# Performance work log

Measured on AMD Instinct MI355X. Metric: run time of the kernel, lower is better.

The kernel has to match this reference:

```python
import jax, jax.numpy as jnp
import numpy as np

B, T_HIST, D, H, STEPS = 2048, 15, 64, 128, 20
MAX_STEPS = 48           # max adaptive steps per unit time interval
DT0, RTOL, ATOL = 0.1, 1e-3, 1e-6
SAFETY, FMIN, FMAX = 0.9, 0.2, 10.0

# Tsit5 (Tsitouras 2011) tableau
A21 = 0.161
A31, A32 = -0.008480655492356989, 0.335480655492357
A41, A42, A43 = 2.8971530571054935, -6.359448489975075, 4.3622954328695815
A51, A52, A53, A54 = 5.325864828439257, -11.748883564062828, 7.4955393428898365, -0.09249506636175525
A61, A62, A63, A64, A65 = 5.86145544294642, -12.92096931784711, 8.159367898576159, -0.071584973281401, -0.028269050394068383
B1, B2, B3, B4, B5, B6 = 0.09646076681806523, 0.01, 0.4798896504144996, 1.379008574103742, -3.290069515436081, 2.324710524099774
E1, E2, E3, E4, E5, E6, E7 = (-0.00178001105222577714, -0.0008164344596567469, 0.007880878010261995,
                              -0.1447110071732629, 0.5823571654525552, -0.45808210592918697, 0.015151515151515152)


def _mlp(y, W1, b1, W2, b2, W3, b3):
    h = jax.nn.softplus(y @ W1.T + b1)
    h = jax.nn.softplus(h @ W2.T + b2)
    return h @ W3.T + b3


def _solve(y0, W1, b1, W2, b2, W3, b3, steps):
    f = lambda y: _mlp(y, W1, b1, W2, b2, W3, b3)  # batched vector field [B,D]->[B,D]
    Bn = y0.shape[0]

    def segment(carry, t1):
        y, dt = carry
        t = jnp.full((Bn,), t1 - 1.0, y0.dtype)
        done = jnp.zeros((Bn,), bool)

        def body(state, _):
            t, y, dt, done = state
            dt_c = jnp.minimum(dt, t1 - t)          # clip to segment end
            h = dt_c[:, None]
            k1 = f(y)
            k2 = f(y + h * (A21 * k1))
            k3 = f(y + h * (A31 * k1 + A32 * k2))
            k4 = f(y + h * (A41 * k1 + A42 * k2 + A43 * k3))
            k5 = f(y + h * (A51 * k1 + A52 * k2 + A53 * k3 + A54 * k4))
            k6 = f(y + h * (A61 * k1 + A62 * k2 + A63 * k3 + A64 * k4 + A65 * k5))
            y5 = y + h * (B1 * k1 + B2 * k2 + B3 * k3 + B4 * k4 + B5 * k5 + B6 * k6)
            k7 = f(y5)
            err = h * (E1 * k1 + E2 * k2 + E3 * k3 + E4 * k4 + E5 * k5 + E6 * k6 + E7 * k7)
            scale = ATOL + RTOL * jnp.maximum(jnp.abs(y), jnp.abs(y5))
            err_norm = jnp.sqrt(jnp.mean((err / scale) ** 2, axis=-1))  # [B]
            accept = (err_norm <= 1.0) & (~done)
            factor = jnp.clip(SAFETY * jnp.maximum(err_norm, 1e-10) ** (-0.2), FMIN, FMAX)
            t_new = jnp.where(accept, t + dt_c, t)
            y_new = jnp.where(accept[:, None], y5, y)
            dt_new = jnp.where(done, dt, dt_c * factor)
            done_new = done | (t_new >= t1 - 1e-8)
            return (t_new, y_new, dt_new, done_new), None

        (t, y, dt, done), _ = jax.lax.scan(jax.checkpoint(body), (t, y, dt, done), None, length=MAX_STEPS)
        return (y, dt), y

    ts1 = jnp.arange(1, steps + 1, dtype=y0.dtype)
    dt0 = jnp.full((Bn,), DT0, y0.dtype)
    (_, _), ys = jax.lax.scan(segment, (y0, dt0), ts1)  # ys: [steps, B, D]
    return jnp.transpose(ys, (1, 0, 2))                  # [B, steps, D]


def setup_inputs() -> dict:
    key = jax.random.key(0)
    ks = jax.random.split(key, 7)
    history = jax.random.normal(ks[0], (B, T_HIST, D), jnp.float32)
    # small-scale init keeps the vector field mild so adaptive steps converge
    W1 = jax.random.normal(ks[1], (H, D), jnp.float32) * (0.5 / np.sqrt(D))
    b1 = jax.random.normal(ks[2], (H,), jnp.float32) * 0.05
    W2 = jax.random.normal(ks[3], (H, H), jnp.float32) * (0.5 / np.sqrt(H))
    b2 = jax.random.normal(ks[4], (H,), jnp.float32) * 0.05
    W3 = jax.random.normal(ks[5], (D, H), jnp.float32) * (0.1 / np.sqrt(H))
    b3 = jax.random.normal(ks[6], (D,), jnp.float32) * 0.05
    return {"history": history, "W1": W1, "b1": b1, "W2": W2, "b2": b2, "W3": W3, "b3": b3, "steps": STEPS}


def reference(history, W1, b1, W2, b2, W3, b3, steps):
    y0 = history[:, -1]  # NeuralODE uses only the last history state
    return _solve(y0, W1, b1, W2, b2, W3, b3, steps)
```

## Files before the change

kernel.cpp:

```cpp
#include <hip/hip_runtime.h>
#include <math.h>

#define NB    2048
#define NSEG  20
#define MAXIT 48
#define CH    544
#define BLKS  136

typedef __attribute__((ext_vector_type(8))) short bf8_t;
typedef __attribute__((ext_vector_type(4))) float f32x4;

#define cA21 ((float)0.161)
#define cA31 ((float)-0.008480655492356989)
#define cA32 ((float)0.335480655492357)
#define cA41 ((float)2.8971530571054935)
#define cA42 ((float)-6.359448489975075)
#define cA43 ((float)4.3622954328695815)
#define cA51 ((float)5.325864828439257)
#define cA52 ((float)-11.748883564062828)
#define cA53 ((float)7.4955393428898365)
#define cA54 ((float)-0.09249506636175525)
#define cA61 ((float)5.86145544294642)
#define cA62 ((float)-12.92096931784711)
#define cA63 ((float)8.159367898576159)
#define cA64 ((float)-0.071584973281401)
#define cA65 ((float)-0.028269050394068383)
#define cB1  ((float)0.09646076681806523)
#define cB2  ((float)0.01)
#define cB3  ((float)0.4798896504144996)
#define cB4  ((float)1.379008574103742)
#define cB5  ((float)-3.290069515436081)
#define cB6  ((float)2.324710524099774)
#define cE1  ((float)-0.001780011052225777)
#define cE2  ((float)-0.0008164344596567469)
#define cE3  ((float)0.007880878010261995)
#define cE4  ((float)-0.1447110071732629)
#define cE5  ((float)0.5823571654525552)
#define cE6  ((float)-0.45808210592918697)
#define cE7  ((float)0.015151515151515152)

__device__ __forceinline__ void split2(float x, short &hi, short &lo) {
    unsigned u = __float_as_uint(x);
    hi = (short)(u >> 16);
    float r = x - __uint_as_float(u & 0xFFFF0000u);
    lo = (short)(__float_as_uint(r) >> 16);
}

__device__ __forceinline__ float softplus_f(float x) {
    float t = exp2f(-fabsf(x) * 1.442695040888963f);
    return fmaxf(x, 0.0f) + log2f(1.0f + t) * 0.6931471805599453f;
}

__device__ __forceinline__ unsigned pk(short a, short b) {
    return ((unsigned)(unsigned short)a) | (((unsigned)(unsigned short)b) << 16);
}

__device__ __forceinline__ float fold8(float x) {
    int r = __builtin_amdgcn_update_dpp(__float_as_int(x), __float_as_int(x),
                                        0x128, 0xF, 0xF, false);
    return x + __int_as_float(r);
}

__global__ __launch_bounds__(512)
void ode_kernel(const float* __restrict__ history,
                const float* __restrict__ W1, const float* __restrict__ b1,
                const float* __restrict__ W2, const float* __restrict__ b2,
                const float* __restrict__ W3, const float* __restrict__ b3,
                float* __restrict__ out)
{
    __shared__ alignas(16) short argB[2 * CH];
    __shared__ alignas(16) short h1B[4 * CH];
    __shared__ alignas(16) short h2B[4 * CH];
    __shared__ float rrP[32];

    const int tid  = threadIdx.x;
    const int wave = tid >> 6, lane = tid & 63;
    const int quad = lane >> 4, col = lane & 15;
    const int jb   = 16 * wave + 4 * quad;

    bf8_t A1h[2], A1l[2], A2h[4], A2l[4], A3h[4], A3l[4];
#pragma unroll
    for (int c = 0; c < 2; ++c) {
        const float* p = W1 + (size_t)(16 * wave + col) * 64 + 32 * c + 8 * quad;
        bf8_t h, l;
#pragma unroll
        for (int j = 0; j < 8; ++j) { short hs, ls; split2(p[j], hs, ls); h[j] = hs; l[j] = ls; }
        A1h[c] = h; A1l[c] = l;
    }
#pragma unroll
    for (int c = 0; c < 4; ++c) {
        const float* p = W2 + (size_t)(16 * wave + col) * 128 + 32 * c + 8 * quad;
        bf8_t h, l;
#pragma unroll
        for (int j = 0; j < 8; ++j) { short hs, ls; split2(p[j], hs, ls); h[j] = hs; l[j] = ls; }
        A2h[c] = h; A2l[c] = l;
    }
    const int esel = col >> 3;
    const int e    = col & 7;
    const int d0   = 16 * wave + 4 * quad + 2 * esel;
    const size_t elemIdx = (size_t)(blockIdx.x * 8 + e);

    float b3v0 = 0.f, b3v1 = 0.f;
    if (wave < 4) {
#pragma unroll
        for (int c = 0; c < 4; ++c) {
            const float* p = W3 + (size_t)(16 * wave + col) * 128 + 32 * c + 8 * quad;
            bf8_t h, l;
#pragma unroll
            for (int j = 0; j < 8; ++j) { short hs, ls; split2(p[j], hs, ls); h[j] = hs; l[j] = ls; }
            A3h[c] = h; A3l[c] = l;
        }
        b3v0 = b3[d0]; b3v1 = b3[d0 + 1];
    } else {
        bf8_t z = {0, 0, 0, 0, 0, 0, 0, 0};
#pragma unroll
        for (int c = 0; c < 4; ++c) { A3h[c] = z; A3l[c] = z; }
    }
    const f32x4 b1f = *(const f32x4*)(b1 + jb);
    const f32x4 b2f = *(const f32x4*)(b2 + jb);

    const int ai = (d0 >> 5) * CH + ((d0 >> 3) & 3) * BLKS + e * 8 + (d0 & 7);

    const int j0    = 16 * wave + 4 * quad + 2 * esel;
    const int epidx = (j0 >> 5) * CH + ((j0 >> 3) & 3) * BLKS + e * 8 + (j0 & 7);

    const int boff = quad * BLKS + col * 8;

    auto gemm = [&](const bf8_t* Ah, const bf8_t* Al, const short* Bc, int nch) -> f32x4 {
        f32x4 a0 = {0.f, 0.f, 0.f, 0.f}, a1 = a0;
#pragma unroll
        for (int c = 0; c < nch; ++c) {
            bf8_t b = *(const bf8_t*)(Bc + c * CH + boff);
            a0 = __builtin_amdgcn_mfma_f32_16x16x32_bf16(Ah[c], b, a0, 0, 0, 0);
            a1 = __builtin_amdgcn_mfma_f32_16x16x32_bf16(Al[c], b, a1, 0, 0, 0);
        }
        f32x4 s;
#pragma unroll
        for (int r = 0; r < 4; ++r) s[r] = a0[r] + a1[r];
        return s;
    };

    auto epi = [&](f32x4 s, f32x4 bias, short* Bn) {
        float t0 = fold8(s[0]) + bias[0];
        float t1 = fold8(s[1]) + bias[1];
        float t2 = fold8(s[2]) + bias[2];
        float t3 = fold8(s[3]) + bias[3];
        float x0 = esel ? t2 : t0;
        float x1 = esel ? t3 : t1;
        float p0 = softplus_f(x0), p1 = softplus_f(x1);
        short h0, l0, h1, l1;
        split2(p0, h0, l0);
        split2(p1, h1, l1);
        *(unsigned*)(Bn + epidx)      = pk(h0, h1);
        *(unsigned*)(Bn + epidx + 64) = pk(l0, l1);
    };

    auto eval = [&](float &kv0, float &kv1) {
        __syncthreads();
        f32x4 s1 = gemm(A1h, A1l, argB, 2);
        epi(s1, b1f, h1B);
        __syncthreads();
        f32x4 s2 = gemm(A2h, A2l, h1B, 4);
        epi(s2, b2f, h2B);
        __syncthreads();
        if (wave < 4) {
            f32x4 s3 = gemm(A3h, A3l, h2B, 4);
            float f0 = fold8(s3[0]);
            float f1 = fold8(s3[1]);
            float f2 = fold8(s3[2]);
            float f3 = fold8(s3[3]);
            kv0 = (esel ? f2 : f0) + b3v0;
            kv1 = (esel ? f3 : f1) + b3v1;
        }
    };

    float y0 = 0.f, y1 = 0.f;
    float dt = 0.1f;
    float k1a = 0.f, k1b = 0.f, k2a, k2b, k3a, k3b, k4a, k4b, k5a, k5b, k6a, k6b;

    if (wave < 4) {
        float2 yy = *(const float2*)(history + (elemIdx * 15 + 14) * 64 + d0);
        y0 = yy.x; y1 = yy.y;
        short h0, l0, h1, l1;
        split2(y0, h0, l0); split2(y1, h1, l1);
        *(unsigned*)(argB + ai)      = pk(h0, h1);
        *(unsigned*)(argB + ai + 64) = pk(l0, l1);
    }
    eval(k1a, k1b);

#pragma unroll 1
    for (int seg = 1; seg <= NSEG; ++seg) {
        const float t1 = (float)seg;
        float t = t1 - 1.0f;
        bool done = false;

#pragma unroll 1
        for (int it = 0; it < MAXIT; ++it) {
            const float dt_c = fminf(dt, t1 - t);
            const float h = dt_c;
            float y50 = 0.f, y51 = 0.f, k7a = 0.f, k7b = 0.f;

#pragma unroll 1
            for (int st = 2; st <= 7; ++st) {
                if (wave < 4) {
                    float sum0, sum1;
                    switch (st) {
                        case 2: sum0 = cA21 * k1a;
                                sum1 = cA21 * k1b; break;
                        case 3: sum0 = fmaf(cA31, k1a, cA32 * k2a);
                                sum1 = fmaf(cA31, k1b, cA32 * k2b); break;
                        case 4: sum0 = fmaf(cA41, k1a, fmaf(cA42, k2a, cA43 * k3a));
                                sum1 = fmaf(cA41, k1b, fmaf(cA42, k2b, cA43 * k3b)); break;
                        case 5: sum0 = fmaf(cA51, k1a, fmaf(cA52, k2a, fmaf(cA53, k3a, cA54 * k4a)));
                                sum1 = fmaf(cA51, k1b, fmaf(cA52, k2b, fmaf(cA53, k3b, cA54 * k4b))); break;
                        case 6: sum0 = fmaf(cA61, k1a, fmaf(cA62, k2a, fmaf(cA63, k3a, fmaf(cA64, k4a, cA65 * k5a))));
                                sum1 = fmaf(cA61, k1b, fmaf(cA62, k2b, fmaf(cA63, k3b, fmaf(cA64, k4b, cA65 * k5b)))); break;
                        default: sum0 = fmaf(cB1, k1a, fmaf(cB2, k2a, fmaf(cB3, k3a, fmaf(cB4, k4a, fmaf(cB5, k5a, cB6 * k6a)))));
                                 sum1 = fmaf(cB1, k1b, fmaf(cB2, k2b, fmaf(cB3, k3b, fmaf(cB4, k4b, fmaf(cB5, k5b, cB6 * k6b))))); break;
                    }
                    float arg0 = fmaf(h, sum0, y0);
                    float arg1 = fmaf(h, sum1, y1);
                    if (st == 7) { y50 = arg0; y51 = arg1; }
                    short h0, l0, h1, l1;
                    split2(arg0, h0, l0); split2(arg1, h1, l1);
                    *(unsigned*)(argB + ai)      = pk(h0, h1);
                    *(unsigned*)(argB + ai + 64) = pk(l0, l1);
                }
                float kv0 = 0.f, kv1 = 0.f;
                eval(kv0, kv1);
                if (wave < 4) {
                    switch (st) {
                        case 2: k2a = kv0; k2b = kv1; break;
                        case 3: k3a = kv0; k3b = kv1; break;
                        case 4: k4a = kv0; k4b = kv1; break;
                        case 5: k5a = kv0; k5b = kv1; break;
                        case 6: k6a = kv0; k6b = kv1; break;
                        default: k7a = kv0; k7b = kv1; break;
                    }
                }
            }

            float rr2 = 0.f;
            if (wave < 4) {
                float es0 = fmaf(cE1, k1a, fmaf(cE2, k2a, fmaf(cE3, k3a,
                            fmaf(cE4, k4a, fmaf(cE5, k5a, fmaf(cE6, k6a, cE7 * k7a))))));
                float es1 = fmaf(cE1, k1b, fmaf(cE2, k2b, fmaf(cE3, k3b,
                            fmaf(cE4, k4b, fmaf(cE5, k5b, fmaf(cE6, k6b, cE7 * k7b))))));
                float err0 = h * es0, err1 = h * es1;
                float sc0 = fmaf(1e-3f, fmaxf(fabsf(y0), fabsf(y50)), 1e-6f);
                float sc1 = fmaf(1e-3f, fmaxf(fabsf(y1), fabsf(y51)), 1e-6f);
                float r0 = err0 / sc0, r1 = err1 / sc1;
                rr2 = fmaf(r0, r0, r1 * r1);
            }
            rr2 += __shfl_xor(rr2, 16, 64);
            rr2 += __shfl_xor(rr2, 32, 64);
            rr2 = fold8(rr2);
            if (wave < 4 && lane < 8) rrP[wave * 8 + lane] = rr2;
            __syncthreads();
            float rs = ((rrP[e] + rrP[8 + e]) + rrP[16 + e]) + rrP[24 + e];
            float en = sqrtf(rs * (1.0f / 64.0f));

            bool accept = (en <= 1.0f) && !done;
            float fac = 0.9f * exp2f(-0.2f * log2f(fmaxf(en, 1e-10f)));
            fac = fminf(fmaxf(fac, 0.2f), 10.0f);

            if (wave < 4 && accept) { y0 = y50; y1 = y51; k1a = k7a; k1b = k7b; }
            if (accept) t += dt_c;
            if (!done) dt = dt_c * fac;
            done = done || (t >= t1 - 1e-8f);
            if (__all(done)) break;
        }

        if (wave < 4) {
            float2 yy; yy.x = y0; yy.y = y1;
            *(float2*)(out + (elemIdx * NSEG + (seg - 1)) * 64 + d0) = yy;
        }
    }
}

extern "C" void kernel_launch(void* const* d_in, const int* in_sizes, int n_in,
                              void* d_out, int out_size, void* d_ws, size_t ws_size,
                              hipStream_t stream) {
    const float* history = (const float*)d_in[0];
    const float* W1 = (const float*)d_in[1];
    const float* b1 = (const float*)d_in[2];
    const float* W2 = (const float*)d_in[3];
    const float* b2 = (const float*)d_in[4];
    const float* W3 = (const float*)d_in[5];
    const float* b3 = (const float*)d_in[6];
    float* out = (float*)d_out;

    ode_kernel<<<dim3(NB / 8), dim3(512), 0, stream>>>(history, W1, b1, W2, b2, W3, b3, out);
}
```

Measured before the change: 278.7 us.

## Fold first-layer GEMM into last layer via precomputed W1·W3 product

```diff
diff --git a/kernel.cpp b/kernel.cpp
--- a/kernel.cpp
+++ b/kernel.cpp
@@ -68,7 +68,6 @@
                 const float* __restrict__ W3, const float* __restrict__ b3,
                 float* __restrict__ out)
 {
-    __shared__ alignas(16) short argB[2 * CH];
     __shared__ alignas(16) short h1B[4 * CH];
     __shared__ alignas(16) short h2B[4 * CH];
     __shared__ float rrP[32];
@@ -77,16 +76,14 @@
     const int wave = tid >> 6, lane = tid & 63;
     const int quad = lane >> 4, col = lane & 15;
     const int jb   = 16 * wave + 4 * quad;
-
-    bf8_t A1h[2], A1l[2], A2h[4], A2l[4], A3h[4], A3l[4];
-#pragma unroll
-    for (int c = 0; c < 2; ++c) {
-        const float* p = W1 + (size_t)(16 * wave + col) * 64 + 32 * c + 8 * quad;
-        bf8_t h, l;
-#pragma unroll
-        for (int j = 0; j < 8; ++j) { short hs, ls; split2(p[j], hs, ls); h[j] = hs; l[j] = ls; }
-        A1h[c] = h; A1l[c] = l;
-    }
+    const int esel = col >> 3;
+    const int e    = col & 7;
+    const int j0   = jb + 2 * esel;
+    const size_t elemIdx = (size_t)(blockIdx.x * 8 + e);
+    const int zi   = (j0 >> 5) * CH + ((j0 >> 3) & 3) * BLKS + e * 8 + (j0 & 7);
+    const int boff = quad * BLKS + col * 8;
+
+    bf8_t A2h[4], A2l[4];
 #pragma unroll
     for (int c = 0; c < 4; ++c) {
         const float* p = W2 + (size_t)(16 * wave + col) * 128 + 32 * c + 8 * quad;
@@ -95,11 +92,7 @@
         for (int j = 0; j < 8; ++j) { short hs, ls; split2(p[j], hs, ls); h[j] = hs; l[j] = ls; }
         A2h[c] = h; A2l[c] = l;
     }
-    const int esel = col >> 3;
-    const int e    = col & 7;
-    const int d0   = 16 * wave + 4 * quad + 2 * esel;
-    const size_t elemIdx = (size_t)(blockIdx.x * 8 + e);
-
+    bf8_t A3h[4], A3l[4];
     float b3v0 = 0.f, b3v1 = 0.f;
     if (wave < 4) {
 #pragma unroll
@@ -110,21 +103,46 @@
             for (int j = 0; j < 8; ++j) { short hs, ls; split2(p[j], hs, ls); h[j] = hs; l[j] = ls; }
             A3h[c] = h; A3l[c] = l;
         }
-        b3v0 = b3[d0]; b3v1 = b3[d0 + 1];
+        b3v0 = b3[j0]; b3v1 = b3[j0 + 1];
     } else {
         bf8_t z = {0, 0, 0, 0, 0, 0, 0, 0};
 #pragma unroll
         for (int c = 0; c < 4; ++c) { A3h[c] = z; A3l[c] = z; }
     }
-    const f32x4 b1f = *(const f32x4*)(b1 + jb);
     const f32x4 b2f = *(const f32x4*)(b2 + jb);
-
-    const int ai = (d0 >> 5) * CH + ((d0 >> 3) & 3) * BLKS + e * 8 + (d0 & 7);
-
-    const int j0    = 16 * wave + 4 * quad + 2 * esel;
-    const int epidx = (j0 >> 5) * CH + ((j0 >> 3) & 3) * BLKS + e * 8 + (j0 & 7);
-
-    const int boff = quad * BLKS + col * 8;
+    const float b1v0 = b1[j0], b1v1 = b1[j0 + 1];
+
+    bf8_t Mh[4], Ml[4];
+    {
+        float accM[4][8];
+#pragma unroll
+        for (int cc = 0; cc < 4; ++cc)
+#pragma unroll
+            for (int j = 0; j < 8; ++j) accM[cc][j] = 0.f;
+        const float* w1r = W1 + (size_t)(16 * wave + col) * 64;
+#pragma unroll 2
+        for (int d = 0; d < 64; ++d) {
+            float wv = w1r[d];
+            const float* w3r = W3 + (size_t)d * 128 + 8 * quad;
+#pragma unroll
+            for (int cc = 0; cc < 4; ++cc) {
+                f32x4 va = *(const f32x4*)(w3r + 32 * cc);
+                f32x4 vb = *(const f32x4*)(w3r + 32 * cc + 4);
+#pragma unroll
+                for (int j = 0; j < 4; ++j) {
+                    accM[cc][j]     = fmaf(wv, va[j], accM[cc][j]);
+                    accM[cc][4 + j] = fmaf(wv, vb[j], accM[cc][4 + j]);
+                }
+            }
+        }
+#pragma unroll
+        for (int cc = 0; cc < 4; ++cc) {
+            bf8_t hh, ll;
+#pragma unroll
+            for (int j = 0; j < 8; ++j) { short hs, ls; split2(accM[cc][j], hs, ls); hh[j] = hs; ll[j] = ls; }
+            Mh[cc] = hh; Ml[cc] = ll;
+        }
+    }
 
     auto gemm = [&](const bf8_t* Ah, const bf8_t* Al, const short* Bc, int nch) -> f32x4 {
         f32x4 a0 = {0.f, 0.f, 0.f, 0.f}, a1 = a0;
@@ -139,6 +157,41 @@
         for (int r = 0; r < 4; ++r) s[r] = a0[r] + a1[r];
         return s;
     };
+
+    float zy0, zy1, cc0, cc1;
+    float ys0 = 0.f, ys1 = 0.f;
+    {
+        bf8_t W1h[2], W1l[2];
+#pragma unroll
+        for (int c = 0; c < 2; ++c) {
+            const float* p = W1 + (size_t)(16 * wave + col) * 64 + 32 * c + 8 * quad;
+            bf8_t h, l;
+#pragma unroll
+            for (int j = 0; j < 8; ++j) { short hs, ls; split2(p[j], hs, ls); h[j] = hs; l[j] = ls; }
+            W1h[c] = h; W1l[c] = l;
+        }
+        if (wave < 4) {
+            float2 yy = *(const float2*)(history + (elemIdx * 15 + 14) * 64 + j0);
+            ys0 = yy.x; ys1 = yy.y;
+            short ha, la, hb, lb;
+            split2(ys0, ha, la); split2(ys1, hb, lb);
+            *(unsigned*)(h1B + zi)      = pk(ha, hb);
+            *(unsigned*)(h1B + zi + 64) = pk(la, lb);
+            split2(b3v0, ha, la); split2(b3v1, hb, lb);
+            *(unsigned*)(h2B + zi)      = pk(ha, hb);
+            *(unsigned*)(h2B + zi + 64) = pk(la, lb);
+        }
+        __syncthreads();
+        f32x4 sz = gemm(W1h, W1l, h1B, 2);
+        f32x4 sc = gemm(W1h, W1l, h2B, 2);
+        float f0 = fold8(sz[0]), f1 = fold8(sz[1]), f2 = fold8(sz[2]), f3 = fold8(sz[3]);
+        zy0 = (esel ? f2 : f0) + b1v0;
+        zy1 = (esel ? f3 : f1) + b1v1;
+        float g0 = fold8(sc[0]), g1 = fold8(sc[1]), g2 = fold8(sc[2]), g3 = fold8(sc[3]);
+        cc0 = esel ? g2 : g0;
+        cc1 = esel ? g3 : g1;
+        __syncthreads();
+    }
 
     auto epi = [&](f32x4 s, f32x4 bias, short* Bn) {
         float t0 = fold8(s[0]) + bias[0];
@@ -148,45 +201,53 @@
         float x0 = esel ? t2 : t0;
         float x1 = esel ? t3 : t1;
         float p0 = softplus_f(x0), p1 = softplus_f(x1);
-        short h0, l0, h1, l1;
-        split2(p0, h0, l0);
-        split2(p1, h1, l1);
-        *(unsigned*)(Bn + epidx)      = pk(h0, h1);
-        *(unsigned*)(Bn + epidx + 64) = pk(l0, l1);
+        short h0s, l0s, h1s, l1s;
+        split2(p0, h0s, l0s);
+        split2(p1, h1s, l1s);
+        *(unsigned*)(Bn + zi)      = pk(h0s, h1s);
+        *(unsigned*)(Bn + zi + 64) = pk(l0s, l1s);
     };
 
-    auto eval = [&](float &kv0, float &kv1) {
-        __syncthreads();
-        f32x4 s1 = gemm(A1h, A1l, argB, 2);
-        epi(s1, b1f, h1B);
+    auto do_eval = [&](float za, float zb, float &ua, float &ub, float &ka, float &kb) {
+        float p0 = softplus_f(za), p1 = softplus_f(zb);
+        short h0s, l0s, h1s, l1s;
+        split2(p0, h0s, l0s);
+        split2(p1, h1s, l1s);
+        *(unsigned*)(h1B + zi)      = pk(h0s, h1s);
+        *(unsigned*)(h1B + zi + 64) = pk(l0s, l1s);
         __syncthreads();
         f32x4 s2 = gemm(A2h, A2l, h1B, 4);
         epi(s2, b2f, h2B);
         __syncthreads();
-        if (wave < 4) {
-            f32x4 s3 = gemm(A3h, A3l, h2B, 4);
-            float f0 = fold8(s3[0]);
-            float f1 = fold8(s3[1]);
-            float f2 = fold8(s3[2]);
-            float f3 = fold8(s3[3]);
-            kv0 = (esel ? f2 : f0) + b3v0;
-            kv1 = (esel ? f3 : f1) + b3v1;
-        }
+        f32x4 zz = {0.f, 0.f, 0.f, 0.f};
+        f32x4 m0 = zz, m1 = zz, w0 = zz, w1 = zz;
+#pragma unroll
+        for (int c = 0; c < 4; ++c) {
+            bf8_t b = *(const bf8_t*)(h2B + c * CH + boff);
+            m0 = __builtin_amdgcn_mfma_f32_16x16x32_bf16(Mh[c],  b, m0, 0, 0, 0);
+            m1 = __builtin_amdgcn_mfma_f32_16x16x32_bf16(Ml[c],  b, m1, 0, 0, 0);
+            w0 = __builtin_amdgcn_mfma_f32_16x16x32_bf16(A3h[c], b, w0, 0, 0, 0);
+            w1 = __builtin_amdgcn_mfma_f32_16x16x32_bf16(A3l[c], b, w1, 0, 0, 0);
+        }
+        float f0 = fold8(m0[0] + m1[0]);
+        float f1 = fold8(m0[1] + m1[1]);
+        float f2 = fold8(m0[2] + m1[2]);
+        float f3 = fold8(m0[3] + m1[3]);
+        ua = (esel ? f2 : f0) + cc0;
+        ub = (esel ? f3 : f1) + cc1;
+        float g0 = fold8(w0[0] + w1[0]);
+        float g1 = fold8(w0[1] + w1[1]);
+        float g2 = fold8(w0[2] + w1[2]);
+        float g3 = fold8(w0[3] + w1[3]);
+        ka = (esel ? g2 : g0) + b3v0;
+        kb = (esel ? g3 : g1) + b3v1;
     };
 
-    float y0 = 0.f, y1 = 0.f;
     float dt = 0.1f;
+    float u1a, u1b, u2a, u2b, u3a, u3b, u4a, u4b, u5a, u5b, u6a, u6b;
     float k1a = 0.f, k1b = 0.f, k2a, k2b, k3a, k3b, k4a, k4b, k5a, k5b, k6a, k6b;
 
-    if (wave < 4) {
-        float2 yy = *(const float2*)(history + (elemIdx * 15 + 14) * 64 + d0);
-        y0 = yy.x; y1 = yy.y;
-        short h0, l0, h1, l1;
-        split2(y0, h0, l0); split2(y1, h1, l1);
-        *(unsigned*)(argB + ai)      = pk(h0, h1);
-        *(unsigned*)(argB + ai + 64) = pk(l0, l1);
-    }
-    eval(k1a, k1b);
+    do_eval(zy0, zy1, u1a, u1b, k1a, k1b);
 
 #pragma unroll 1
     for (int seg = 1; seg <= NSEG; ++seg) {
@@ -199,44 +260,43 @@
             const float dt_c = fminf(dt, t1 - t);
             const float h = dt_c;
             float y50 = 0.f, y51 = 0.f, k7a = 0.f, k7b = 0.f;
+            float u7a = 0.f, u7b = 0.f, zy5a = 0.f, zy5b = 0.f;
 
 #pragma unroll 1
             for (int st = 2; st <= 7; ++st) {
-                if (wave < 4) {
-                    float sum0, sum1;
-                    switch (st) {
-                        case 2: sum0 = cA21 * k1a;
-                                sum1 = cA21 * k1b; break;
-                        case 3: sum0 = fmaf(cA31, k1a, cA32 * k2a);
-                                sum1 = fmaf(cA31, k1b, cA32 * k2b); break;
-                        case 4: sum0 = fmaf(cA41, k1a, fmaf(cA42, k2a, cA43 * k3a));
-                                sum1 = fmaf(cA41, k1b, fmaf(cA42, k2b, cA43 * k3b)); break;
-                        case 5: sum0 = fmaf(cA51, k1a, fmaf(cA52, k2a, fmaf(cA53, k3a, cA54 * k4a)));
-                                sum1 = fmaf(cA51, k1b, fmaf(cA52, k2b, fmaf(cA53, k3b, cA54 * k4b))); break;
-                        case 6: sum0 = fmaf(cA61, k1a, fmaf(cA62, k2a, fmaf(cA63, k3a, fmaf(cA64, k4a, cA65 * k5a))));
-                                sum1 = fmaf(cA61, k1b, fmaf(cA62, k2b, fmaf(cA63, k3b, fmaf(cA64, k4b, cA65 * k5b)))); break;
-                        default: sum0 = fmaf(cB1, k1a, fmaf(cB2, k2a, fmaf(cB3, k3a, fmaf(cB4, k4a, fmaf(cB5, k5a, cB6 * k6a)))));
-                                 sum1 = fmaf(cB1, k1b, fmaf(cB2, k2b, fmaf(cB3, k3b, fmaf(cB4, k4b, fmaf(cB5, k5b, cB6 * k6b))))); break;
-                    }
-                    float arg0 = fmaf(h, sum0, y0);
-                    float arg1 = fmaf(h, sum1, y1);
-                    if (st == 7) { y50 = arg0; y51 = arg1; }
-                    short h0, l0, h1, l1;
-                    split2(arg0, h0, l0); split2(arg1, h1, l1);
-                    *(unsigned*)(argB + ai)      = pk(h0, h1);
-                    *(unsigned*)(argB + ai + 64) = pk(l0, l1);
+                float sa, sb;
+                switch (st) {
+                    case 2: sa = cA21 * u1a;
+                            sb = cA21 * u1b; break;
+                    case 3: sa = fmaf(cA31, u1a, cA32 * u2a);
+                            sb = fmaf(cA31, u1b, cA32 * u2b); break;
+                    case 4: sa = fmaf(cA41, u1a, fmaf(cA42, u2a, cA43 * u3a));
+                            sb = fmaf(cA41, u1b, fmaf(cA42, u2b, cA43 * u3b)); break;
+                    case 5: sa = fmaf(cA51, u1a, fmaf(cA52, u2a, fmaf(cA53, u3a, cA54 * u4a)));
+                            sb = fmaf(cA51, u1b, fmaf(cA52, u2b, fmaf(cA53, u3b, cA54 * u4b))); break;
+                    case 6: sa = fmaf(cA61, u1a, fmaf(cA62, u2a, fmaf(cA63, u3a, fmaf(cA64, u4a, cA65 * u5a))));
+                            sb = fmaf(cA61, u1b, fmaf(cA62, u2b, fmaf(cA63, u3b, fmaf(cA64, u4b, cA65 * u5b)))); break;
+                    default: sa = fmaf(cB1, u1a, fmaf(cB2, u2a, fmaf(cB3, u3a, fmaf(cB4, u4a, fmaf(cB5, u5a, cB6 * u6a)))));
+                             sb = fmaf(cB1, u1b, fmaf(cB2, u2b, fmaf(cB3, u3b, fmaf(cB4, u4b, fmaf(cB5, u5b, cB6 * u6b))))); break;
                 }
-                float kv0 = 0.f, kv1 = 0.f;
-                eval(kv0, kv1);
-                if (wave < 4) {
-                    switch (st) {
-                        case 2: k2a = kv0; k2b = kv1; break;
-                        case 3: k3a = kv0; k3b = kv1; break;
-                        case 4: k4a = kv0; k4b = kv1; break;
-                        case 5: k5a = kv0; k5b = kv1; break;
-                        case 6: k6a = kv0; k6b = kv1; break;
-                        default: k7a = kv0; k7b = kv1; break;
-                    }
+                float za = fmaf(h, sa, zy0);
+                float zb = fmaf(h, sb, zy1);
+                if (st == 7) {
+                    zy5a = za; zy5b = zb;
+                    float ta = fmaf(cB1, k1a, fmaf(cB2, k2a, fmaf(cB3, k3a, fmaf(cB4, k4a, fmaf(cB5, k5a, cB6 * k6a)))));
+                    float tb = fmaf(cB1, k1b, fmaf(cB2, k2b, fmaf(cB3, k3b, fmaf(cB4, k4b, fmaf(cB5, k5b, cB6 * k6b)))));
+                    y50 = fmaf(h, ta, ys0);
+                    y51 = fmaf(h, tb, ys1);
+                }
+                float ua, ub, ka, kb;
+                do_eval(za, zb, ua, ub, ka, kb);
+                switch (st) {
+                    case 2: u2a = ua; u2b = ub; k2a = ka; k2b = kb; break;
+                    case 3: u3a = ua; u3b = ub; k3a = ka; k3b = kb; break;
+                    case 4: u4a = ua; u4b = ub; k4a = ka; k4b = kb; break;
+                    case 5: u5a = ua; u5b = ub; k5a = ka; k5b = kb; break;
+                    case 6: u6a = ua; u6b = ub; k6a = ka; k6b = kb; break;
+                    default: u7a = ua; u7b = ub; k7a = ka; k7b = kb; break;
                 }
             }
 
@@ -247,8 +307,8 @@
                 float es1 = fmaf(cE1, k1b, fmaf(cE2, k2b, fmaf(cE3, k3b,
                             fmaf(cE4, k4b, fmaf(cE5, k5b, fmaf(cE6, k6b, cE7 * k7b))))));
                 float err0 = h * es0, err1 = h * es1;
-                float sc0 = fmaf(1e-3f, fmaxf(fabsf(y0), fabsf(y50)), 1e-6f);
-                float sc1 = fmaf(1e-3f, fmaxf(fabsf(y1), fabsf(y51)), 1e-6f);
+                float sc0 = fmaf(1e-3f, fmaxf(fabsf(ys0), fabsf(y50)), 1e-6f);
+                float sc1 = fmaf(1e-3f, fmaxf(fabsf(ys1), fabsf(y51)), 1e-6f);
                 float r0 = err0 / sc0, r1 = err1 / sc1;
                 rr2 = fmaf(r0, r0, r1 * r1);
             }
@@ -264,16 +324,20 @@
             float fac = 0.9f * exp2f(-0.2f * log2f(fmaxf(en, 1e-10f)));
             fac = fminf(fmaxf(fac, 0.2f), 10.0f);
 
-            if (wave < 4 && accept) { y0 = y50; y1 = y51; k1a = k7a; k1b = k7b; }
-            if (accept) t += dt_c;
+            if (accept) {
+                t += dt_c;
+                zy0 = zy5a; zy1 = zy5b;
+                u1a = u7a;  u1b = u7b;
+                if (wave < 4) { ys0 = y50; ys1 = y51; k1a = k7a; k1b = k7b; }
+            }
             if (!done) dt = dt_c * fac;
             done = done || (t >= t1 - 1e-8f);
             if (__all(done)) break;
         }
 
         if (wave < 4) {
-            float2 yy; yy.x = y0; yy.y = y1;
-            *(float2*)(out + (elemIdx * NSEG + (seg - 1)) * 64 + d0) = yy;
+            float2 yy; yy.x = ys0; yy.y = ys1;
+            *(float2*)(out + (elemIdx * NSEG + (seg - 1)) * 64 + j0) = yy;
         }
     }
 }
```

Result: slower. 307.4 us (+10.3%).

## Flatten segment and step loops so each element advances across segments independently

Applied to the files above, without the earlier changes.

```diff
diff --git a/kernel.cpp b/kernel.cpp
--- a/kernel.cpp
+++ b/kernel.cpp
@@ -148,11 +148,11 @@
         float x0 = esel ? t2 : t0;
         float x1 = esel ? t3 : t1;
         float p0 = softplus_f(x0), p1 = softplus_f(x1);
-        short h0, l0, h1, l1;
-        split2(p0, h0, l0);
-        split2(p1, h1, l1);
-        *(unsigned*)(Bn + epidx)      = pk(h0, h1);
-        *(unsigned*)(Bn + epidx + 64) = pk(l0, l1);
+        short h0s, l0s, h1s, l1s;
+        split2(p0, h0s, l0s);
+        split2(p1, h1s, l1s);
+        *(unsigned*)(Bn + epidx)      = pk(h0s, h1s);
+        *(unsigned*)(Bn + epidx + 64) = pk(l0s, l1s);
     };
 
     auto eval = [&](float &kv0, float &kv1) {
@@ -174,107 +174,111 @@
         }
     };
 
+    auto argw = [&](float a0, float a1) {
+        short h0s, l0s, h1s, l1s;
+        split2(a0, h0s, l0s); split2(a1, h1s, l1s);
+        *(unsigned*)(argB + ai)      = pk(h0s, h1s);
+        *(unsigned*)(argB + ai + 64) = pk(l0s, l1s);
+    };
+
     float y0 = 0.f, y1 = 0.f;
-    float dt = 0.1f;
     float k1a = 0.f, k1b = 0.f, k2a, k2b, k3a, k3b, k4a, k4b, k5a, k5b, k6a, k6b;
+
+    float dt   = 0.1f;
+    float t    = 0.0f;
+    int   segE = 1;
+    bool  aliveE = true;
 
     if (wave < 4) {
         float2 yy = *(const float2*)(history + (elemIdx * 15 + 14) * 64 + d0);
         y0 = yy.x; y1 = yy.y;
-        short h0, l0, h1, l1;
-        split2(y0, h0, l0); split2(y1, h1, l1);
-        *(unsigned*)(argB + ai)      = pk(h0, h1);
-        *(unsigned*)(argB + ai + 64) = pk(l0, l1);
+        argw(y0, y1);
     }
     eval(k1a, k1b);
 
 #pragma unroll 1
-    for (int seg = 1; seg <= NSEG; ++seg) {
-        const float t1 = (float)seg;
-        float t = t1 - 1.0f;
-        bool done = false;
+    for (int iter = 0; iter < NSEG * MAXIT; ++iter) {
+        const float tEnd = (float)segE;
+        const float dt_c = fminf(dt, tEnd - t);
+        const float h = dt_c;
+        float y50 = 0.f, y51 = 0.f, k7a = 0.f, k7b = 0.f;
 
 #pragma unroll 1
-        for (int it = 0; it < MAXIT; ++it) {
-            const float dt_c = fminf(dt, t1 - t);
-            const float h = dt_c;
-            float y50 = 0.f, y51 = 0.f, k7a = 0.f, k7b = 0.f;
-
-#pragma unroll 1
-            for (int st = 2; st <= 7; ++st) {
-                if (wave < 4) {
-                    float sum0, sum1;
-                    switch (st) {
-                        case 2: sum0 = cA21 * k1a;
-                                sum1 = cA21 * k1b; break;
-                        case 3: sum0 = fmaf(cA31, k1a, cA32 * k2a);
-                                sum1 = fmaf(cA31, k1b, cA32 * k2b); break;
-                        case 4: sum0 = fmaf(cA41, k1a, fmaf(cA42, k2a, cA43 * k3a));
-                                sum1 = fmaf(cA41, k1b, fmaf(cA42, k2b, cA43 * k3b)); break;
-                        case 5: sum0 = fmaf(cA51, k1a, fmaf(cA52, k2a, fmaf(cA53, k3a, cA54 * k4a)));
-                                sum1 = fmaf(cA51, k1b, fmaf(cA52, k2b, fmaf(cA53, k3b, cA54 * k4b))); break;
-                        case 6: sum0 = fmaf(cA61, k1a, fmaf(cA62, k2a, fmaf(cA63, k3a, fmaf(cA64, k4a, cA65 * k5a))));
-                                sum1 = fmaf(cA61, k1b, fmaf(cA62, k2b, fmaf(cA63, k3b, fmaf(cA64, k4b, cA65 * k5b)))); break;
-                        default: sum0 = fmaf(cB1, k1a, fmaf(cB2, k2a, fmaf(cB3, k3a, fmaf(cB4, k4a, fmaf(cB5, k5a, cB6 * k6a)))));
-                                 sum1 = fmaf(cB1, k1b, fmaf(cB2, k2b, fmaf(cB3, k3b, fmaf(cB4, k4b, fmaf(cB5, k5b, cB6 * k6b))))); break;
-                    }
-                    float arg0 = fmaf(h, sum0, y0);
-                    float arg1 = fmaf(h, sum1, y1);
-                    if (st == 7) { y50 = arg0; y51 = arg1; }
-                    short h0, l0, h1, l1;
-                    split2(arg0, h0, l0); split2(arg1, h1, l1);
-                    *(unsigned*)(argB + ai)      = pk(h0, h1);
-                    *(unsigned*)(argB + ai + 64) = pk(l0, l1);
+        for (int st = 2; st <= 7; ++st) {
+            if (wave < 4) {
+                float sum0, sum1;
+                switch (st) {
+                    case 2: sum0 = cA21 * k1a;
+                            sum1 = cA21 * k1b; break;
+                    case 3: sum0 = fmaf(cA31, k1a, cA32 * k2a);
+                            sum1 = fmaf(cA31, k1b, cA32 * k2b); break;
+                    case 4: sum0 = fmaf(cA41, k1a, fmaf(cA42, k2a, cA43 * k3a));
+                            sum1 = fmaf(cA41, k1b, fmaf(cA42, k2b, cA43 * k3b)); break;
+                    case 5: sum0 = fmaf(cA51, k1a, fmaf(cA52, k2a, fmaf(cA53, k3a, cA54 * k4a)));
+                            sum1 = fmaf(cA51, k1b, fmaf(cA52, k2b, fmaf(cA53, k3b, cA54 * k4b))); break;
+                    case 6: sum0 = fmaf(cA61, k1a, fmaf(cA62, k2a, fmaf(cA63, k3a, fmaf(cA64, k4a, cA65 * k5a))));
+                            sum1 = fmaf(cA61, k1b, fmaf(cA62, k2b, fmaf(cA63, k3b, fmaf(cA64, k4b, cA65 * k5b)))); break;
+                    default: sum0 = fmaf(cB1, k1a, fmaf(cB2, k2a, fmaf(cB3, k3a, fmaf(cB4, k4a, fmaf(cB5, k5a, cB6 * k6a)))));
+                             sum1 = fmaf(cB1, k1b, fmaf(cB2, k2b, fmaf(cB3, k3b, fmaf(cB4, k4b, fmaf(cB5, k5b, cB6 * k6b))))); break;
                 }
-                float kv0 = 0.f, kv1 = 0.f;
-                eval(kv0, kv1);
-                if (wave < 4) {
-                    switch (st) {
-                        case 2: k2a = kv0; k2b = kv1; break;
-                        case 3: k3a = kv0; k3b = kv1; break;
-                        case 4: k4a = kv0; k4b = kv1; break;
-                        case 5: k5a = kv0; k5b = kv1; break;
-                        case 6: k6a = kv0; k6b = kv1; break;
-                        default: k7a = kv0; k7b = kv1; break;
-                    }
+                float arg0 = fmaf(h, sum0, y0);
+                float arg1 = fmaf(h, sum1, y1);
+                if (st == 7) { y50 = arg0; y51 = arg1; }
+                argw(arg0, arg1);
+            }
+            float kv0 = 0.f, kv1 = 0.f;
+            eval(kv0, kv1);
+            if (wave < 4) {
+                switch (st) {
+                    case 2: k2a = kv0; k2b = kv1; break;
+                    case 3: k3a = kv0; k3b = kv1; break;
+                    case 4: k4a = kv0; k4b = kv1; break;
+                    case 5: k5a = kv0; k5b = kv1; break;
+                    case 6: k6a = kv0; k6b = kv1; break;
+                    default: k7a = kv0; k7b = kv1; break;
                 }
             }
-
-            float rr2 = 0.f;
-            if (wave < 4) {
-                float es0 = fmaf(cE1, k1a, fmaf(cE2, k2a, fmaf(cE3, k3a,
-                            fmaf(cE4, k4a, fmaf(cE5, k5a, fmaf(cE6, k6a, cE7 * k7a))))));
-                float es1 = fmaf(cE1, k1b, fmaf(cE2, k2b, fmaf(cE3, k3b,
-                            fmaf(cE4, k4b, fmaf(cE5, k5b, fmaf(cE6, k6b, cE7 * k7b))))));
-                float err0 = h * es0, err1 = h * es1;
-                float sc0 = fmaf(1e-3f, fmaxf(fabsf(y0), fabsf(y50)), 1e-6f);
-                float sc1 = fmaf(1e-3f, fmaxf(fabsf(y1), fabsf(y51)), 1e-6f);
-                float r0 = err0 / sc0, r1 = err1 / sc1;
-                rr2 = fmaf(r0, r0, r1 * r1);
+        }
+
+        float rr2 = 0.f;
+        if (wave < 4) {
+            float es0 = fmaf(cE1, k1a, fmaf(cE2, k2a, fmaf(cE3, k3a,
+                        fmaf(cE4, k4a, fmaf(cE5, k5a, fmaf(cE6, k6a, cE7 * k7a))))));
+            float es1 = fmaf(cE1, k1b, fmaf(cE2, k2b, fmaf(cE3, k3b,
+                        fmaf(cE4, k4b, fmaf(cE5, k5b, fmaf(cE6, k6b, cE7 * k7b))))));
+            float err0 = h * es0, err1 = h * es1;
+            float sc0 = fmaf(1e-3f, fmaxf(fabsf(y0), fabsf(y50)), 1e-6f);
+            float sc1 = fmaf(1e-3f, fmaxf(fabsf(y1), fabsf(y51)), 1e-6f);
+            float r0 = err0 / sc0, r1 = err1 / sc1;
+            rr2 = fmaf(r0, r0, r1 * r1);
+        }
+        rr2 += __shfl_xor(rr2, 16, 64);
+        rr2 += __shfl_xor(rr2, 32, 64);
+        rr2 = fold8(rr2);
+        if (wave < 4 && lane < 8) rrP[wave * 8 + lane] = rr2;
+        __syncthreads();
+        float rs = ((rrP[e] + rrP[8 + e]) + rrP[16 + e]) + rrP[24 + e];
+        float en = sqrtf(rs * (1.0f / 64.0f));
+
+        bool accept = (en <= 1.0f) && aliveE;
+        float fac = 0.9f * exp2f(-0.2f * log2f(fmaxf(en, 1e-10f)));
+        fac = fminf(fmaxf(fac, 0.2f), 10.0f);
+
+        if (wave < 4 && accept) { y0 = y50; y1 = y51; k1a = k7a; k1b = k7b; }
+        if (aliveE) dt = dt_c * fac;
+        if (accept) {
+            t += dt_c;
+            if (t >= tEnd - 1e-8f) {
+                if (wave < 4) {
+                    float2 yy; yy.x = y0; yy.y = y1;
+                    *(float2*)(out + (elemIdx * NSEG + (segE - 1)) * 64 + d0) = yy;
+                }
+                t = tEnd;
+                segE += 1;
+                if (segE > NSEG) aliveE = false;
             }
-            rr2 += __shfl_xor(rr2, 16, 64);
-            rr2 += __shfl_xor(rr2, 32, 64);
-            rr2 = fold8(rr2);
-            if (wave < 4 && lane < 8) rrP[wave * 8 + lane] = rr2;
-            __syncthreads();
-            float rs = ((rrP[e] + rrP[8 + e]) + rrP[16 + e]) + rrP[24 + e];
-            float en = sqrtf(rs * (1.0f / 64.0f));
-
-            bool accept = (en <= 1.0f) && !done;
-            float fac = 0.9f * exp2f(-0.2f * log2f(fmaxf(en, 1e-10f)));
-            fac = fminf(fmaxf(fac, 0.2f), 10.0f);
-
-            if (wave < 4 && accept) { y0 = y50; y1 = y51; k1a = k7a; k1b = k7b; }
-            if (accept) t += dt_c;
-            if (!done) dt = dt_c * fac;
-            done = done || (t >= t1 - 1e-8f);
-            if (__all(done)) break;
-        }
-
-        if (wave < 4) {
-            float2 yy; yy.x = y0; yy.y = y1;
-            *(float2*)(out + (elemIdx * NSEG + (seg - 1)) * 64 + d0) = yy;
-        }
+        }
+        if (__all(!aliveE)) break;
     }
 }
 
```

After: 278.1 us. About the same (-0.2%).
